# Kernel tuning notes

Measured on AMD Instinct MI355X. Metric: run time of the kernel, lower is better.

Reference implementation:

```python
import jax, jax.numpy as jnp
import numpy as np

D_MODEL, D_K, D_V = 1024, 64, 64

def setup_inputs() -> dict:
    key = jax.random.key(0)
    ks = jax.random.split(key, 7)
    s = 1.0 / np.sqrt(D_MODEL)
    return {
        "x": jax.random.normal(ks[0], (4, 4096, D_MODEL), dtype=jnp.float32),
        "w_q": jax.random.normal(ks[1], (D_MODEL, D_K), dtype=jnp.float32) * s,
        "b_q": jnp.zeros((D_K,), dtype=jnp.float32),
        "w_k": jax.random.normal(ks[2], (D_MODEL, D_K), dtype=jnp.float32) * s,
        "b_k": jnp.zeros((D_K,), dtype=jnp.float32),
        "w_v": jax.random.normal(ks[3], (D_MODEL, D_V), dtype=jnp.float32) * s,
        "b_v": jnp.zeros((D_V,), dtype=jnp.float32),
    }

def reference(x, w_q, b_q, w_k, b_k, w_v, b_v):
    # x: [b, s, d_model]
    q = x @ w_q + b_q                      # [b, s, d_k]
    k = x @ w_k + b_k                      # [b, s, d_k]
    v = x @ w_v + b_v                      # [b, s, d_v]
    scores = jnp.einsum("bqd,bkd->bqk", q, k) / jnp.sqrt(jnp.float32(D_K))
    seq_len = scores.shape[-1]
    causal = jnp.tril(jnp.ones((seq_len, seq_len), dtype=bool))  # keep lower-tri
    scores = jnp.where(causal, scores, -jnp.inf)
    probs = jax.nn.softmax(scores, axis=-1)
    return jnp.einsum("bqk,bkd->bqd", probs, v)  # [b, s, d_v]
```

## Files before the change

kernel.cpp:

```cpp
#include <hip/hip_runtime.h>
#include <hip/hip_bf16.h>

using f32x4    = __attribute__((ext_vector_type(4))) float;
using f32x16   = __attribute__((ext_vector_type(16))) float;
using bf16x8   = __attribute__((ext_vector_type(8))) __bf16;
using ushort8  = __attribute__((ext_vector_type(8))) unsigned short;
using ushort4v = __attribute__((ext_vector_type(4))) unsigned short;
using uint4v   = __attribute__((ext_vector_type(4))) unsigned int;
using float4v  = __attribute__((ext_vector_type(4))) float;

#define LOG2E 1.44269504088896340736f
#define SHIFT_L2 5.77078016355585f

static __device__ __forceinline__ unsigned short f2bf(float f) {
  union { __hip_bfloat16 h; unsigned short u; } cv;
  cv.h = __float2bfloat16(f);
  return cv.u;
}
static __device__ __forceinline__ bf16x8 ld_bf8_g(const void* p) {
  ushort8 u = *(const ushort8*)p;
  return __builtin_bit_cast(bf16x8, u);
}
static __device__ __forceinline__ float fast_exp2(float x) {
#if __has_builtin(__builtin_amdgcn_exp2f)
  return __builtin_amdgcn_exp2f(x);
#else
  return exp2f(x);
#endif
}
static __device__ __forceinline__ unsigned int pk2(float a, float b) {
  return (unsigned int)f2bf(a) | ((unsigned int)f2bf(b) << 16);
}

__global__ __launch_bounds__(256) void wprep_kernel(
    const float* __restrict__ wq, const float* __restrict__ wk,
    const float* __restrict__ wv, unsigned short* __restrict__ Wt) {
  int idx = blockIdx.x * 256 + threadIdx.x;
  int col = idx >> 10;
  int k   = idx & 1023;
  const float* w = (col < 64) ? wq : (col < 128) ? wk : wv;
  int c = col & 63;
  Wt[idx] = f2bf(w[k * 64 + c]);
}

__global__ __launch_bounds__(256) void proj_kernel(
    const float* __restrict__ x, const unsigned short* __restrict__ Wt,
    const float* __restrict__ bq, const float* __restrict__ bk,
    const float* __restrict__ bv,
    unsigned short* __restrict__ qb, unsigned short* __restrict__ kreg,
    unsigned short* __restrict__ vreg) {
  __shared__ __align__(16) char As[32 * 128];
  __shared__ __align__(16) char Bs[192 * 128];
  int tid = threadIdx.x, wave = tid >> 6, lane = tid & 63;
  int rowBase = blockIdx.x * 32;
  int rhalf = (wave & 1) * 16;
  int chalf = (wave >> 1) * 96;
  int l15 = lane & 15, lh = lane >> 4;

  f32x4 zero4 = {0.f, 0.f, 0.f, 0.f};
  f32x4 acc[6];
#pragma unroll
  for (int i = 0; i < 6; ++i) acc[i] = zero4;

  for (int kt = 0; kt < 16; ++kt) {
    int k0 = kt * 64;
    {
      int row = tid >> 3, c0 = (tid & 7) * 8;
      const float4v* src = (const float4v*)(x + (size_t)(rowBase + row) * 1024 + k0 + c0);
      float4v f0 = src[0], f1 = src[1];
      ushort8 u;
#pragma unroll
      for (int e = 0; e < 4; ++e) { u[e] = f2bf(f0[e]); u[4 + e] = f2bf(f1[e]); }
      *(ushort8*)(As + ((row * 128 + c0 * 2) ^ ((row & 7) << 4))) = u;
    }
#pragma unroll
    for (int i = 0; i < 6; ++i) {
      int c = tid + 256 * i;
      int col = c >> 3, kc = c & 7;
      ushort8 v = *(const ushort8*)(Wt + (size_t)col * 1024 + k0 + kc * 8);
      *(ushort8*)(Bs + ((col * 128 + kc * 16) ^ ((col & 7) << 4))) = v;
    }
    __syncthreads();
    bf16x8 a[2];
#pragma unroll
    for (int ks = 0; ks < 2; ++ks) {
      int row = rhalf + l15;
      a[ks] = ld_bf8_g(As + ((row * 128 + ks * 64 + lh * 16) ^ ((row & 7) << 4)));
    }
#pragma unroll
    for (int cf = 0; cf < 6; ++cf) {
      int col = chalf + cf * 16 + l15;
#pragma unroll
      for (int ks = 0; ks < 2; ++ks) {
        bf16x8 b = ld_bf8_g(Bs + ((col * 128 + ks * 64 + lh * 16) ^ ((col & 7) << 4)));
        acc[cf] = __builtin_amdgcn_mfma_f32_16x16x32_bf16(a[ks], b, acc[cf], 0, 0, 0);
      }
    }
    __syncthreads();
  }
#pragma unroll
  for (int cf = 0; cf < 6; ++cf) {
    int col = chalf + cf * 16 + l15;
    int sel = col >> 6, c64 = col & 63;
    const float* bias = (sel == 0) ? bq : (sel == 1) ? bk : bv;
    float bb = bias[c64];
    if (sel == 0) {
#pragma unroll
      for (int r = 0; r < 4; ++r) {
        int row = rowBase + rhalf + lh * 4 + r;
        qb[(size_t)row * 64 + c64] = f2bf((acc[cf][r] + bb) * (0.125f * LOG2E));
      }
    } else if (sel == 1) {
      int j16 = c64 >> 4, hik = (c64 >> 3) & 1, e = c64 & 7;
#pragma unroll
      for (int r = 0; r < 4; ++r) {
        int s = rowBase + rhalf + lh * 4 + r;
        int b = s >> 12, sl = s & 4095;
        int ch = sl >> 7, kvw = sl & 127;
        int kvq = kvw >> 5, lk = kvw & 31;
        size_t off = (((size_t)(b * 32 + ch)) << 14) + kvq * 4096 + j16 * 1024 +
                     (hik * 32 + lk) * 16 + e * 2;
        *(unsigned short*)((char*)kreg + off) = f2bf(acc[cf][r] + bb);
      }
    } else {
      ushort4v w;
#pragma unroll
      for (int r = 0; r < 4; ++r) w[r] = f2bf(acc[cf][r] + bb);
      int s0 = rowBase + rhalf + lh * 4;
      int b = s0 >> 12, sl = s0 & 4095;
      int ch = sl >> 7, kvw = sl & 127;
      int kvq = kvw >> 5, k5 = kvw & 31;
      int kj = k5 >> 4, hiv = (k5 >> 3) & 1, e0 = k5 & 7;
      int dt = c64 >> 5, lv = c64 & 31, f = kj * 2 + dt;
      size_t off = (((size_t)(b * 32 + ch)) << 14) + kvq * 4096 + f * 1024 +
                   (hiv * 32 + lv) * 16 + e0 * 2;
      *(ushort4v*)((char*)vreg + off) = w;
    }
  }
}

__global__ __launch_bounds__(64, 4) void attn_kernel(
    const unsigned short* __restrict__ qb, const unsigned short* __restrict__ kreg,
    const unsigned short* __restrict__ vreg, float* __restrict__ po,
    float* __restrict__ lo) {
  int lane = threadIdx.x & 63;
  int l31 = lane & 31, hi = lane >> 5;
  int wid = blockIdx.x;
  int T = 127 - (wid >> 5);
  int low = wid & 31;
  int batch = low & 3, ph = low >> 2;
  int Tq = T * 32;
  const size_t bO = (size_t)batch * 262144;
  const char* kb = (const char*)kreg + ((size_t)batch << 19);
  const char* vb = (const char*)vreg + ((size_t)batch << 19);

  const unsigned short* qp = qb + bO + (size_t)(Tq + l31) * 64 + hi * 8;
  bf16x8 qf0 = ld_bf8_g(qp);
  bf16x8 qf1 = ld_bf8_g(qp + 16);
  bf16x8 qf2 = ld_bf8_g(qp + 32);
  bf16x8 qf3 = ld_bf8_g(qp + 48);

  f32x16 o0, o1;
#pragma unroll
  for (int r = 0; r < 16; ++r) { o0[r] = 0.f; o1[r] = 0.f; }
  float lsum = 0.f;

#pragma unroll 1
  for (int st = ph; st <= T; st += 8) {
    size_t base = ((size_t)(st >> 2) << 14) + (st & 3) * 4096 + lane * 16;
    const char* kp = kb + base;
    const char* vp = vb + base;
    bf16x8 k0 = ld_bf8_g(kp);
    bf16x8 k1 = ld_bf8_g(kp + 1024);
    bf16x8 k2 = ld_bf8_g(kp + 2048);
    bf16x8 k3 = ld_bf8_g(kp + 3072);
    bf16x8 v0 = ld_bf8_g(vp);
    bf16x8 v1 = ld_bf8_g(vp + 1024);
    bf16x8 v2 = ld_bf8_g(vp + 2048);
    bf16x8 v3 = ld_bf8_g(vp + 3072);

    f32x16 sc;
#pragma unroll
    for (int r = 0; r < 16; ++r) sc[r] = 0.f;
    sc = __builtin_amdgcn_mfma_f32_32x32x16_bf16(k0, qf0, sc, 0, 0, 0);
    sc = __builtin_amdgcn_mfma_f32_32x32x16_bf16(k1, qf1, sc, 0, 0, 0);
    sc = __builtin_amdgcn_mfma_f32_32x32x16_bf16(k2, qf2, sc, 0, 0, 0);
    sc = __builtin_amdgcn_mfma_f32_32x32x16_bf16(k3, qf3, sc, 0, 0, 0);
    if (st == T) {
      int qg = Tq + l31;
#pragma unroll
      for (int r = 0; r < 16; ++r) {
        int kvg = 32 * st + (r & 3) + 8 * (r >> 2) + 4 * hi;
        if (kvg > qg) sc[r] = -3.0e38f;
      }
    }
    float pv[16];
#pragma unroll
    for (int r = 0; r < 16; ++r) {
      pv[r] = fast_exp2(sc[r] - SHIFT_L2);
      lsum += pv[r];
    }
#pragma unroll
    for (int kj = 0; kj < 2; ++kj) {
      const int R = 8 * kj;
      unsigned int A0 = pk2(pv[R + 0], pv[R + 1]);
      unsigned int A1 = pk2(pv[R + 2], pv[R + 3]);
      unsigned int B0 = pk2(pv[R + 4], pv[R + 5]);
      unsigned int B1 = pk2(pv[R + 6], pv[R + 7]);
      unsigned int s0 = hi ? A0 : B0;
      unsigned int s1 = hi ? A1 : B1;
      unsigned int r0 = __shfl_xor((int)s0, 32, 64);
      unsigned int r1 = __shfl_xor((int)s1, 32, 64);
      uint4v dw = {hi ? r0 : A0, hi ? r1 : A1, hi ? B0 : r0, hi ? B1 : r1};
      bf16x8 pa = __builtin_bit_cast(bf16x8, dw);
      if (kj == 0) {
        o0 = __builtin_amdgcn_mfma_f32_32x32x16_bf16(pa, v0, o0, 0, 0, 0);
        o1 = __builtin_amdgcn_mfma_f32_32x32x16_bf16(pa, v1, o1, 0, 0, 0);
      } else {
        o0 = __builtin_amdgcn_mfma_f32_32x32x16_bf16(pa, v2, o0, 0, 0, 0);
        o1 = __builtin_amdgcn_mfma_f32_32x32x16_bf16(pa, v3, o1, 0, 0, 0);
      }
    }
  }

  lsum += __shfl_xor(lsum, 32, 64);

  float* pdst = po + (size_t)ph * 1048576 + bO + (size_t)Tq * 64;
#pragma unroll
  for (int r = 0; r < 16; ++r) {
    int qloc = (r & 3) + 8 * (r >> 2) + 4 * hi;
    pdst[qloc * 64 + l31] = o0[r];
    pdst[qloc * 64 + 32 + l31] = o1[r];
  }
  if (hi == 0) lo[ph * 16384 + batch * 4096 + Tq + l31] = lsum;
}

__global__ __launch_bounds__(256) void merge_kernel(
    const float* __restrict__ po, const float* __restrict__ lo,
    float* __restrict__ out) {
  int i = blockIdx.x * 256 + threadIdx.x;
  int row = i >> 4;
  float4v a = ((const float4v*)po)[i];
  float L = lo[row];
#pragma unroll
  for (int ph = 1; ph < 8; ++ph) {
    a += ((const float4v*)po)[i + ph * 262144];
    L += lo[row + ph * 16384];
  }
  a *= (1.0f / L);
  ((float4v*)out)[i] = a;
}

extern "C" void kernel_launch(void* const* d_in, const int* in_sizes, int n_in,
                              void* d_out, int out_size, void* d_ws, size_t ws_size,
                              hipStream_t stream) {
  const float* x  = (const float*)d_in[0];
  const float* wq = (const float*)d_in[1];
  const float* bq = (const float*)d_in[2];
  const float* wk = (const float*)d_in[3];
  const float* bk = (const float*)d_in[4];
  const float* wv = (const float*)d_in[5];
  const float* bv = (const float*)d_in[6];

  unsigned short* Wt   = (unsigned short*)d_ws;
  unsigned short* qbuf = Wt + 192 * 1024;
  unsigned short* kreg = qbuf + 16384 * 64;
  unsigned short* vreg = kreg + 16384 * 64;
  float*          po   = (float*)(vreg + 16384 * 64);
  float*          lo   = po + 8 * 1048576;

  wprep_kernel<<<768, 256, 0, stream>>>(wq, wk, wv, Wt);
  proj_kernel<<<512, 256, 0, stream>>>(x, Wt, bq, bk, bv, qbuf, kreg, vreg);
  attn_kernel<<<4096, 64, 0, stream>>>(qbuf, kreg, vreg, po, lo);
  merge_kernel<<<1024, 256, 0, stream>>>(po, lo, (float*)d_out);
}
```

Before: 57.02 us.

## Pre-swizzle weights into MFMA fragment layout and pipeline projection loads

The weight prep kernel now writes bf16 weights in per-lane MFMA fragment order, so the projection kernel loads B operands straight from global memory into registers instead of staging them through shared memory. The x tile is double-buffered in shared memory and prefetched in registers two steps ahead, with one barrier per k-step instead of two. This removes most LDS traffic and sync overhead in the projection, at the cost of higher register pressure from the 24 B fragment registers, with launch bounds set to allow 2 blocks per CU.

```diff
diff --git a/kernel.cpp b/kernel.cpp
--- a/kernel.cpp
+++ b/kernel.cpp
@@ -34,73 +34,100 @@
 
 __global__ __launch_bounds__(256) void wprep_kernel(
     const float* __restrict__ wq, const float* __restrict__ wk,
-    const float* __restrict__ wv, unsigned short* __restrict__ Wt) {
+    const float* __restrict__ wv, unsigned short* __restrict__ Wfrag) {
   int idx = blockIdx.x * 256 + threadIdx.x;
   int col = idx >> 10;
   int k   = idx & 1023;
   const float* w = (col < 64) ? wq : (col < 128) ? wk : wv;
   int c = col & 63;
-  Wt[idx] = f2bf(w[k * 64 + c]);
-}
-
-__global__ __launch_bounds__(256) void proj_kernel(
-    const float* __restrict__ x, const unsigned short* __restrict__ Wt,
+  int n = col >> 4, l15 = col & 15;
+  int kk = k >> 5, lh = (k >> 3) & 3, e = k & 7;
+  size_t elem = ((size_t)(n * 32 + kk) * 64 + lh * 16 + l15) * 8 + e;
+  Wfrag[elem] = f2bf(w[k * 64 + c]);
+}
+
+__global__ __launch_bounds__(256, 2) void proj_kernel(
+    const float* __restrict__ x, const unsigned short* __restrict__ Wfrag,
     const float* __restrict__ bq, const float* __restrict__ bk,
     const float* __restrict__ bv,
     unsigned short* __restrict__ qb, unsigned short* __restrict__ kreg,
     unsigned short* __restrict__ vreg) {
-  __shared__ __align__(16) char As[32 * 128];
-  __shared__ __align__(16) char Bs[192 * 128];
+  __shared__ __align__(16) char As[2][32 * 128];
   int tid = threadIdx.x, wave = tid >> 6, lane = tid & 63;
   int rowBase = blockIdx.x * 32;
   int rhalf = (wave & 1) * 16;
-  int chalf = (wave >> 1) * 96;
+  int nbase = (wave >> 1) * 6;
   int l15 = lane & 15, lh = lane >> 4;
 
-  f32x4 zero4 = {0.f, 0.f, 0.f, 0.f};
+  int arow = tid >> 3, ac0 = (tid & 7) * 8;
+  const float* xp = x + (size_t)(rowBase + arow) * 1024 + ac0;
+  int abyte = (arow * 128 + ac0 * 2) ^ ((arow & 7) << 4);
+  const char* wfb = (const char*)Wfrag + (size_t)lane * 16;
+
   f32x4 acc[6];
 #pragma unroll
-  for (int i = 0; i < 6; ++i) acc[i] = zero4;
-
+  for (int i = 0; i < 6; ++i) acc[i] = (f32x4){0.f, 0.f, 0.f, 0.f};
+
+  float4v aL[2], aH[2];
+  bf16x8 B[2][12];
+
+  aL[0] = *(const float4v*)(xp);
+  aH[0] = *(const float4v*)(xp + 4);
+#pragma unroll
+  for (int j = 0; j < 6; ++j) {
+    B[0][j * 2]     = ld_bf8_g(wfb + (((size_t)(nbase + j) * 32 + 0) << 10));
+    B[0][j * 2 + 1] = ld_bf8_g(wfb + (((size_t)(nbase + j) * 32 + 1) << 10));
+  }
+  {
+    ushort8 u;
+#pragma unroll
+    for (int e = 0; e < 4; ++e) { u[e] = f2bf(aL[0][e]); u[4 + e] = f2bf(aH[0][e]); }
+    *(ushort8*)(As[0] + abyte) = u;
+  }
+  aL[1] = *(const float4v*)(xp + 64);
+  aH[1] = *(const float4v*)(xp + 68);
+  asm volatile("s_waitcnt lgkmcnt(0)" ::: "memory");
+  __builtin_amdgcn_s_barrier();
+  __builtin_amdgcn_sched_barrier(0);
+
+#pragma unroll
   for (int kt = 0; kt < 16; ++kt) {
-    int k0 = kt * 64;
+    const int cur = kt & 1, nxt = cur ^ 1;
+    if (kt < 15) {
+#pragma unroll
+      for (int j = 0; j < 6; ++j) {
+        B[nxt][j * 2]     = ld_bf8_g(wfb + (((size_t)(nbase + j) * 32 + 2 * (kt + 1)) << 10));
+        B[nxt][j * 2 + 1] = ld_bf8_g(wfb + (((size_t)(nbase + j) * 32 + 2 * (kt + 1) + 1) << 10));
+      }
+    }
     {
-      int row = tid >> 3, c0 = (tid & 7) * 8;
-      const float4v* src = (const float4v*)(x + (size_t)(rowBase + row) * 1024 + k0 + c0);
-      float4v f0 = src[0], f1 = src[1];
+      int row = rhalf + l15;
+      bf16x8 a0 = ld_bf8_g(As[cur] + ((row * 128 + lh * 16) ^ ((row & 7) << 4)));
+      bf16x8 a1 = ld_bf8_g(As[cur] + ((row * 128 + 64 + lh * 16) ^ ((row & 7) << 4)));
+#pragma unroll
+      for (int j = 0; j < 6; ++j) {
+        acc[j] = __builtin_amdgcn_mfma_f32_16x16x32_bf16(a0, B[cur][j * 2], acc[j], 0, 0, 0);
+        acc[j] = __builtin_amdgcn_mfma_f32_16x16x32_bf16(a1, B[cur][j * 2 + 1], acc[j], 0, 0, 0);
+      }
+    }
+    if (kt < 15) {
       ushort8 u;
 #pragma unroll
-      for (int e = 0; e < 4; ++e) { u[e] = f2bf(f0[e]); u[4 + e] = f2bf(f1[e]); }
-      *(ushort8*)(As + ((row * 128 + c0 * 2) ^ ((row & 7) << 4))) = u;
-    }
-#pragma unroll
-    for (int i = 0; i < 6; ++i) {
-      int c = tid + 256 * i;
-      int col = c >> 3, kc = c & 7;
-      ushort8 v = *(const ushort8*)(Wt + (size_t)col * 1024 + k0 + kc * 8);
-      *(ushort8*)(Bs + ((col * 128 + kc * 16) ^ ((col & 7) << 4))) = v;
-    }
-    __syncthreads();
-    bf16x8 a[2];
-#pragma unroll
-    for (int ks = 0; ks < 2; ++ks) {
-      int row = rhalf + l15;
-      a[ks] = ld_bf8_g(As + ((row * 128 + ks * 64 + lh * 16) ^ ((row & 7) << 4)));
-    }
-#pragma unroll
-    for (int cf = 0; cf < 6; ++cf) {
-      int col = chalf + cf * 16 + l15;
-#pragma unroll
-      for (int ks = 0; ks < 2; ++ks) {
-        bf16x8 b = ld_bf8_g(Bs + ((col * 128 + ks * 64 + lh * 16) ^ ((col & 7) << 4)));
-        acc[cf] = __builtin_amdgcn_mfma_f32_16x16x32_bf16(a[ks], b, acc[cf], 0, 0, 0);
-      }
-    }
-    __syncthreads();
-  }
+      for (int e = 0; e < 4; ++e) { u[e] = f2bf(aL[nxt][e]); u[4 + e] = f2bf(aH[nxt][e]); }
+      *(ushort8*)(As[nxt] + abyte) = u;
+      if (kt < 14) {
+        aL[cur] = *(const float4v*)(xp + (kt + 2) * 64);
+        aH[cur] = *(const float4v*)(xp + (kt + 2) * 64 + 4);
+      }
+      asm volatile("s_waitcnt lgkmcnt(0)" ::: "memory");
+      __builtin_amdgcn_s_barrier();
+      __builtin_amdgcn_sched_barrier(0);
+    }
+  }
+
 #pragma unroll
   for (int cf = 0; cf < 6; ++cf) {
-    int col = chalf + cf * 16 + l15;
+    int col = (nbase + cf) * 16 + l15;
     int sel = col >> 6, c64 = col & 63;
     const float* bias = (sel == 0) ? bq : (sel == 1) ? bk : bv;
     float bb = bias[c64];
@@ -262,15 +289,15 @@
   const float* wv = (const float*)d_in[5];
   const float* bv = (const float*)d_in[6];
 
-  unsigned short* Wt   = (unsigned short*)d_ws;
-  unsigned short* qbuf = Wt + 192 * 1024;
-  unsigned short* kreg = qbuf + 16384 * 64;
-  unsigned short* vreg = kreg + 16384 * 64;
-  float*          po   = (float*)(vreg + 16384 * 64);
-  float*          lo   = po + 8 * 1048576;
-
-  wprep_kernel<<<768, 256, 0, stream>>>(wq, wk, wv, Wt);
-  proj_kernel<<<512, 256, 0, stream>>>(x, Wt, bq, bk, bv, qbuf, kreg, vreg);
+  unsigned short* Wfrag = (unsigned short*)d_ws;
+  unsigned short* qbuf  = Wfrag + 192 * 1024;
+  unsigned short* kreg  = qbuf + 16384 * 64;
+  unsigned short* vreg  = kreg + 16384 * 64;
+  float*          po    = (float*)(vreg + 16384 * 64);
+  float*          lo    = po + 8 * 1048576;
+
+  wprep_kernel<<<768, 256, 0, stream>>>(wq, wk, wv, Wfrag);
+  proj_kernel<<<512, 256, 0, stream>>>(x, Wfrag, bq, bk, bv, qbuf, kreg, vreg);
   attn_kernel<<<4096, 64, 0, stream>>>(qbuf, kreg, vreg, po, lo);
   merge_kernel<<<1024, 256, 0, stream>>>(po, lo, (float*)d_out);
 }
```

Result: faster. 55.45 us, median of 2 (-2.8%).
